# Kernel tuning notes

Measured on AMD Instinct MI355X. Metric: run time of the kernel, lower is better.

## Reference

```python
import jax, jax.numpy as jnp
import numpy as np

D = 4096      # hidden_size
H = 32        # num_attention_heads
DH = 128      # head_dim
DR = 64       # rope_head_dim (rotated suffix of head_dim)
G = 4         # o_groups
QLR = 1536    # q_lora_rank
OLR = 512     # o_lora_rank
WIN = 2048    # window_size
EPS = 1e-6    # norm_eps
THETA = 10000.0


def rms_norm(x, g):
    return x * jax.lax.rsqrt(jnp.mean(x * x, axis=-1, keepdims=True) + EPS) * g


def rope_interleave(x, cos, sin):
    # interleaved (non-neox) rotary: pairs are adjacent even/odd lanes
    x0, x1 = x[..., 0::2], x[..., 1::2]
    r0 = x0 * cos - x1 * sin
    r1 = x0 * sin + x1 * cos
    return jnp.stack([r0, r1], axis=-1).reshape(x.shape)


def setup_inputs() -> dict:
    ks = jax.random.split(jax.random.key(0), 9)
    B, S = 1, 2048
    return {
        "hidden_states": jax.random.normal(ks[0], (B, S, D), jnp.float32),
        "positions": jnp.arange(S, dtype=jnp.int64),
        "wq_a": jax.random.normal(ks[1], (QLR, D), jnp.float32) * 0.02,
        "q_norm_g": jnp.ones((QLR,), jnp.float32),
        "wq_b": jax.random.normal(ks[2], (H * DH, QLR), jnp.float32) * 0.02,
        "wkv": jax.random.normal(ks[3], (DH, D), jnp.float32) * 0.02,
        "kv_norm_g": jnp.ones((DH,), jnp.float32),
        "wo_a": jax.random.normal(ks[4], (G, OLR, (H * DH) // G), jnp.float32) * 0.02,
        "wo_b": jax.random.normal(ks[5], (D, G * OLR), jnp.float32) * 0.02,
        "attn_sink": jax.random.normal(ks[6], (H,), jnp.float32),
    }


def reference(hidden_states, positions, wq_a, q_norm_g, wq_b, wkv, kv_norm_g, wo_a, wo_b, attn_sink):
    B, S, _ = hidden_states.shape
    # low-rank Q path: wq_a -> RMSNorm -> wq_b -> [B,S,H,DH]
    qr = rms_norm(hidden_states @ wq_a.T, q_norm_g)
    q = (qr @ wq_b.T).reshape(B, S, H, DH)
    # shared latent KV (single head_dim vector, MLA/MQA style): wkv -> RMSNorm
    kv = rms_norm(hidden_states @ wkv.T, kv_norm_g)  # [B,S,DH]
    # rotary tables (interleave mode)
    inv_freq = 1.0 / (THETA ** (jnp.arange(0, DR, 2, dtype=jnp.float32) / DR))
    ang = positions.astype(jnp.float32)[:, None] * inv_freq  # [S, DR/2]
    cos, sin = jnp.cos(ang), jnp.sin(ang)
    # rotate last DR dims of q and k
    q = jnp.concatenate(
        [q[..., : DH - DR], rope_interleave(q[..., DH - DR :], cos[None, :, None, :], sin[None, :, None, :])], -1)
    k = jnp.concatenate(
        [kv[..., : DH - DR], rope_interleave(kv[..., DH - DR :], cos[None, :, :], sin[None, :, :])], -1)
    # windowed causal attention with learned per-head sink logit
    scores = jnp.einsum("bshd,btd->bhst", q, k) * (DH ** -0.5)  # [B,H,S,S]
    i = jnp.arange(S)[:, None]
    j = jnp.arange(S)[None, :]
    mask = (j <= i) & ((i - j) < WIN)
    scores = jnp.where(mask[None, None], scores, jnp.finfo(scores.dtype).min)
    sink = jnp.broadcast_to(attn_sink[None, :, None, None], (B, H, S, 1))
    probs = jax.nn.softmax(jnp.concatenate([scores, sink], axis=-1), axis=-1)[..., :S]
    # value = shared normalized latent (pre-rope)
    out = jnp.einsum("bhst,btd->bshd", probs, kv)  # [B,S,H,DH]
    # grouped low-rank output projection: wo_a per group, then wo_b
    out = out.reshape(B, S, G, (H * DH) // G)
    low = jnp.einsum("bsgd,gkd->bsgk", out, wo_a).reshape(B, S, G * OLR)
    return low @ wo_b.T
```

## Files before the change

kernel.cpp:

```cpp
#include <hip/hip_runtime.h>

typedef unsigned short u16;
typedef __bf16 bf16x8 __attribute__((ext_vector_type(8)));
typedef float  f32x4  __attribute__((ext_vector_type(4)));

#define EPSF 1e-6f

__device__ __forceinline__ u16 f2b(float f) {
  unsigned u = __float_as_uint(f);
  u += 0x7fffu + ((u >> 16) & 1u);
  return (u16)(u >> 16);
}
__device__ __forceinline__ float b2f(u16 u) { return __uint_as_float(((unsigned)u) << 16); }
__device__ __forceinline__ u16 f2bh(float f) { return __builtin_bit_cast(u16, (__bf16)f); }

__device__ __forceinline__ unsigned cvtpk(float lo, float hi) {
  unsigned d;
  asm("v_cvt_pk_bf16_f32 %0, %1, %2" : "=v"(d) : "v"(lo), "v"(hi));
  return d;
}

__device__ __forceinline__ void dma16(const u16* g, u16* l) {
  __builtin_amdgcn_global_load_lds(
      (const __attribute__((address_space(1))) unsigned int*)g,
      (__attribute__((address_space(3))) unsigned int*)l, 16, 0, 0);
}

__global__ void dsv4_cvt(const float* __restrict__ hidden, const float* __restrict__ wq_a,
                         const float* __restrict__ wq_b, const float* __restrict__ wkv,
                         const float* __restrict__ wo_a, const float* __restrict__ wo_b,
                         u16* hb, u16* qab, u16* qbb, u16* kvb, u16* oab, u16* obb)
{
  long c = (long)blockIdx.x * 256 + threadIdx.x;
  const float* s; u16* d; long off;
  if      (c < 1048576) { s = hidden; d = hb;  off = c; }
  else if (c < 1835008) { s = wq_a;   d = qab; off = c - 1048576; }
  else if (c < 2621440) { s = wq_b;   d = qbb; off = c - 1835008; }
  else if (c < 2686976) { s = wkv;    d = kvb; off = c - 2621440; }
  else if (c < 2949120) { s = wo_a;   d = oab; off = c - 2686976; }
  else                  { s = wo_b;   d = obb; off = c - 2949120; }
  const float* p = s + off * 8;
  float4 f0 = *(const float4*)p;
  float4 f1 = *(const float4*)(p + 4);
  union { u16 h[8]; int4 v; } u;
  u.h[0] = f2b(f0.x); u.h[1] = f2b(f0.y); u.h[2] = f2b(f0.z); u.h[3] = f2b(f0.w);
  u.h[4] = f2b(f1.x); u.h[5] = f2b(f1.y); u.h[6] = f2b(f1.z); u.h[7] = f2b(f1.w);
  *(int4*)(d + off * 8) = u.v;
}

template<int BM, bool C_F32>
__global__ __launch_bounds__(256, 2)
void dsv4_gemm(const u16* __restrict__ A, int lda, long sAz,
               const u16* __restrict__ B, int ldb, long sBz,
               void* __restrict__ Cv, int ldc, long sCz,
               int K, int splitTile,
               const u16* __restrict__ Baux, void* __restrict__ Caux, int ldcAux)
{
  constexpr int AJ = BM / 32;
  constexpr int NJ = (BM == 128) ? 4 : 2;
  __shared__ __align__(16) u16 As[2 * BM * 64];
  __shared__ __align__(16) u16 Bs[2 * 128 * 64];

  const int tid   = threadIdx.x;
  const int lane  = tid & 63;
  const int qd    = lane >> 4;
  const int l16   = lane & 15;
  const int wid   = tid >> 6;
  const int wbase = tid & 192;
  const int swz   = l16 & 7;

  int n0 = blockIdx.x * 128;
  const int m0 = blockIdx.y * BM;
  void* Cp = Cv;
  if ((int)blockIdx.x >= splitTile) {
    B = Baux; Cp = Caux; ldc = ldcAux;
    n0 = ((int)blockIdx.x - splitTile) * 128;
  }
  A += (long)blockIdx.z * sAz;
  B += (long)blockIdx.z * sBz;

  const u16* gA[AJ]; u16* lA[AJ];
#pragma unroll
  for (int j = 0; j < AJ; j++) {
    int L = j * 256 + tid, row = L >> 3, c = (L & 7) ^ (row & 7);
    gA[j] = A + (long)(m0 + row) * lda + c * 8;
    lA[j] = As + (j * 256 + wbase) * 8;
  }
  const u16* gB[4]; u16* lB[4];
#pragma unroll
  for (int j = 0; j < 4; j++) {
    int L = j * 256 + tid, row = L >> 3, c = (L & 7) ^ (row & 7);
    gB[j] = B + (long)(n0 + row) * ldb + c * 8;
    lB[j] = Bs + (j * 256 + wbase) * 8;
  }

  f32x4 acc[4][NJ];
#pragma unroll
  for (int i = 0; i < 4; i++)
#pragma unroll
    for (int j = 0; j < NJ; j++) { f32x4 z = {0.f, 0.f, 0.f, 0.f}; acc[i][j] = z; }

  const int wm = (BM == 128) ? (wid >> 1) * 64 : 0;
  const int wn = (BM == 128) ? (wid & 1) * 64 : wid * 32;

  auto issue = [&](int s) {
    const int k  = s << 6;
    const int ab = (s & 1) * (BM * 64);
    const int bb = (s & 1) * (128 * 64);
#pragma unroll
    for (int j = 0; j < AJ; j++) dma16(gA[j] + k, lA[j] + ab);
#pragma unroll
    for (int j = 0; j < 4; j++)  dma16(gB[j] + k, lB[j] + bb);
  };

  const int nsteps = K >> 6;
  issue(0);
  asm volatile("s_waitcnt vmcnt(0)" ::: "memory");
  __builtin_amdgcn_s_barrier();

  for (int t = 0; t < nsteps; t++) {
    if (t + 1 < nsteps) issue(t + 1);
    const int ab = (t & 1) * (BM * 64);
    const int bb = (t & 1) * (128 * 64);

#pragma unroll
    for (int ks2 = 0; ks2 < 2; ks2++) {
      bf16x8 af[4], bg[NJ];
#pragma unroll
      for (int i = 0; i < 4; i++) {
        int row = wm + i * 16 + l16;
        af[i] = *(const bf16x8*)&As[ab + row * 64 + ((((ks2 << 2) + qd) ^ swz) << 3)];
      }
#pragma unroll
      for (int j = 0; j < NJ; j++) {
        int row = wn + j * 16 + l16;
        bg[j] = *(const bf16x8*)&Bs[bb + row * 64 + ((((ks2 << 2) + qd) ^ swz) << 3)];
      }
      __builtin_amdgcn_s_setprio(1);
#pragma unroll
      for (int i = 0; i < 4; i++)
#pragma unroll
        for (int j = 0; j < NJ; j++)
          acc[i][j] = __builtin_amdgcn_mfma_f32_16x16x32_bf16(af[i], bg[j], acc[i][j], 0, 0, 0);
      __builtin_amdgcn_s_setprio(0);
    }

    asm volatile("s_waitcnt lgkmcnt(0)" ::: "memory");
    asm volatile("s_waitcnt vmcnt(0)" ::: "memory");
    __builtin_amdgcn_s_barrier();
  }

#pragma unroll
  for (int i = 0; i < 4; i++)
#pragma unroll
    for (int j = 0; j < NJ; j++)
#pragma unroll
      for (int rr = 0; rr < 4; rr++) {
        long row = m0 + wm + i * 16 + qd * 4 + rr;
        int  col = n0 + wn + j * 16 + l16;
        if (C_F32)
          ((float*)Cp)[row * ldc + col + (long)blockIdx.z * sCz] = acc[i][j][rr];
        else
          ((u16*)Cp)[row * ldc + col + (long)blockIdx.z * sCz] = f2b(acc[i][j][rr]);
      }
}

__global__ void dsv4_rmsnorm(const u16* __restrict__ X, const float* __restrict__ g,
                             u16* __restrict__ Y, int W, float invW)
{
  __shared__ float wsum[4];
  const int row = blockIdx.x;
  const u16* x = X + (long)row * W;
  u16* y = Y + (long)row * W;
  float ss = 0.f;
  for (int i = threadIdx.x; i < W; i += 256) { float v = b2f(x[i]); ss += v * v; }
#pragma unroll
  for (int o = 32; o > 0; o >>= 1) ss += __shfl_xor(ss, o);
  const int wid = threadIdx.x >> 6;
  if ((threadIdx.x & 63) == 0) wsum[wid] = ss;
  __syncthreads();
  float tot = wsum[0] + wsum[1] + wsum[2] + wsum[3];
  float scale = rsqrtf(tot * invW + EPSF);
  for (int i = threadIdx.x; i < W; i += 256)
    y[i] = f2b(b2f(x[i]) * scale * g[i]);
}

__global__ void dsv4_kv_finalize(const u16* __restrict__ KVp, const float* __restrict__ g,
                                 u16* __restrict__ Kout, u16* __restrict__ VTout)
{
  const int wid  = threadIdx.x >> 6;
  const int lane = threadIdx.x & 63;
  const int row  = blockIdx.x * 4 + wid;
  const u16* x = KVp + (long)row * 128;
  float x0 = b2f(x[2 * lane]);
  float x1 = b2f(x[2 * lane + 1]);
  float ss = x0 * x0 + x1 * x1;
#pragma unroll
  for (int o = 32; o > 0; o >>= 1) ss += __shfl_xor(ss, o);
  float scale = rsqrtf(ss * (1.f / 128.f) + EPSF);
  float v0 = x0 * scale * g[2 * lane];
  float v1 = x1 * scale * g[2 * lane + 1];
  VTout[(long)(2 * lane) * 2048 + row]     = f2b(v0);
  VTout[(long)(2 * lane + 1) * 2048 + row] = f2b(v1);
  float k0 = v0, k1 = v1;
  if (lane >= 32) {
    int i = lane - 32;
    float invf = powf(10000.f, -(float)i * (1.f / 32.f));
    float sn, cc;
    sincosf((float)row * invf, &sn, &cc);
    k0 = v0 * cc - v1 * sn;
    k1 = v0 * sn + v1 * cc;
  }
  Kout[(long)row * 128 + 2 * lane]     = f2b(k0);
  Kout[(long)row * 128 + 2 * lane + 1] = f2b(k1);
}

__device__ __forceinline__ void attn_step(
    const bf16x8* qf, bool diag, const u16* __restrict__ KsB,
    const u16* __restrict__ VsB,
    int w, int qd, int l16, int swz, float& m, float& negm, float& l, f32x4* o)
{
  const float scl2 = 0.12754245006257017f;
  const float THRU = 62.0f;
  f32x4 st[4];
#pragma unroll
  for (int i = 0; i < 4; i++) { f32x4 z = {0.f, 0.f, 0.f, 0.f}; st[i] = z; }

  __builtin_amdgcn_s_setprio(1);
#pragma unroll
  for (int ks = 0; ks < 4; ks++) {
#pragma unroll
    for (int nt = 0; nt < 4; nt++) {
      int row = nt * 16 + l16;
      bf16x8 bk = *(const bf16x8*)&KsB[row * 128 + ((((ks << 2) + qd) ^ swz) << 3)];
      st[nt] = __builtin_amdgcn_mfma_f32_16x16x32_bf16(bk, qf[ks], st[nt], 0, 0, 0);
    }
  }
  __builtin_amdgcn_s_setprio(0);

  if (diag) {
#pragma unroll
    for (int nt = 0; nt < 4; nt++)
#pragma unroll
      for (int rr = 0; rr < 4; rr++)
        if ((nt * 16 + qd * 4 + rr) > (w * 16 + l16)) st[nt][rr] = -3.0e38f;
  }

  float t0 = fmaxf(fmaxf(st[0][0], st[0][1]), fmaxf(st[0][2], st[0][3]));
  float t1 = fmaxf(fmaxf(st[1][0], st[1][1]), fmaxf(st[1][2], st[1][3]));
  float t2 = fmaxf(fmaxf(st[2][0], st[2][1]), fmaxf(st[2][2], st[2][3]));
  float t3 = fmaxf(fmaxf(st[3][0], st[3][1]), fmaxf(st[3][2], st[3][3]));
  float t = fmaxf(fmaxf(t0, t1), fmaxf(t2, t3));
  t = fmaxf(t, __shfl_xor(t, 16));
  t = fmaxf(t, __shfl_xor(t, 32));

  if (__any(t > m + THRU)) {
    float mn = fmaxf(m, t);
    float aq = exp2f(scl2 * (m - mn));
    m = mn; negm = -scl2 * mn;
    l *= aq;
    float a4[4];
#pragma unroll
    for (int rr = 0; rr < 4; rr++) a4[rr] = __shfl(aq, qd * 4 + rr);
#pragma unroll
    for (int nt = 0; nt < 8; nt++)
#pragma unroll
      for (int rr = 0; rr < 4; rr++) o[nt][rr] *= a4[rr];
  }

#pragma unroll
  for (int nt = 0; nt < 4; nt++)
#pragma unroll
    for (int rr = 0; rr < 4; rr++) {
      float p = exp2f(fmaf(st[nt][rr], scl2, negm));
      l += p;
      st[nt][rr] = p;
    }

  __builtin_amdgcn_s_setprio(1);
#pragma unroll
  for (int ks = 0; ks < 2; ks++) {
    unsigned A0 = cvtpk(st[2 * ks][0],     st[2 * ks][1]);
    unsigned A1 = cvtpk(st[2 * ks][2],     st[2 * ks][3]);
    unsigned B0 = cvtpk(st[2 * ks + 1][0], st[2 * ks + 1][1]);
    unsigned B1 = cvtpk(st[2 * ks + 1][2], st[2 * ks + 1][3]);
    auto s0 = __builtin_amdgcn_permlane32_swap(A0, B0, false, false);
    auto u0 = __builtin_amdgcn_permlane16_swap(s0[0], s0[1], false, false);
    auto s1 = __builtin_amdgcn_permlane32_swap(A1, B1, false, false);
    auto u1 = __builtin_amdgcn_permlane16_swap(s1[0], s1[1], false, false);
    union { unsigned d[4]; bf16x8 v; } ap;
    ap.d[0] = u0[0]; ap.d[1] = u1[0]; ap.d[2] = u0[1]; ap.d[3] = u1[1];
#pragma unroll
    for (int nt = 0; nt < 8; nt++) {
      int row = nt * 16 + l16;
      bf16x8 bv = *(const bf16x8*)&VsB[row * 64 + ((((ks << 2) + qd) ^ swz) << 3)];
      o[nt] = __builtin_amdgcn_mfma_f32_16x16x32_bf16(ap.v, bv, o[nt], 0, 0, 0);
    }
  }
  __builtin_amdgcn_s_setprio(0);
}

__global__ __launch_bounds__(256, 2)
void dsv4_attn(const u16* __restrict__ Q, const u16* __restrict__ Km,
               const u16* __restrict__ VT, const float* __restrict__ sinkp,
               u16* __restrict__ O)
{
  __shared__ __align__(16) u16 Ks[2][64 * 128];
  __shared__ __align__(16) u16 Vs[2][128 * 64];

  const int b  = blockIdx.x;
  const int h  = blockIdx.y;
  const int qtA = 31 - b, qtB = b;
  const int n1 = qtA + 1, nT = n1 + qtB + 1;
  const int tid  = threadIdx.x;
  const int lane = tid & 63;
  const int w    = tid >> 6;
  const int qd   = lane >> 4;
  const int l16  = lane & 15;
  const int swz  = l16 & 7;

  bf16x8 qfA[4], qfB[4];
#pragma unroll
  for (int t = 0; t < 2; t++) {
    int srow = (t ? qtB : qtA) * 64 + w * 16 + l16;
    const u16* qp = Q + (long)srow * 4096 + h * 128 + qd * 8;
    bf16x8* qf = t ? qfB : qfA;
#pragma unroll
    for (int ks = 0; ks < 4; ks++) {
      union { int4 v; u16 hh[8]; } u;
      u.v = *(const int4*)(qp + ks * 32);
      if (ks >= 2) {
#pragma unroll
        for (int j = 0; j < 4; j++) {
          int i = (ks - 2) * 16 + qd * 4 + j;
          float invf = exp2f((float)i * (-13.287712379549449f / 32.f));
          float sn, cc;
          sincosf((float)srow * invf, &sn, &cc);
          float x0 = b2f(u.hh[2 * j]), x1 = b2f(u.hh[2 * j + 1]);
          u.hh[2 * j]     = f2b(x0 * cc - x1 * sn);
          u.hh[2 * j + 1] = f2b(x0 * sn + x1 * cc);
        }
      }
      qf[ks] = *(bf16x8*)&u;
    }
  }

  const u16* gK[4]; const u16* gV[4]; int lKo[4], lVo[4];
#pragma unroll
  for (int j = 0; j < 4; j++) {
    int cl = j * 256 + tid;
    int krow = cl >> 4, kc = (cl & 15) ^ (krow & 7);
    gK[j] = Km + (long)krow * 128 + kc * 8;
    lKo[j] = (j * 256 + (tid & 192)) * 8;
    int vrow = cl >> 3, vc = (cl & 7) ^ (vrow & 7);
    gV[j] = VT + (long)vrow * 2048 + vc * 8;
    lVo[j] = (j * 256 + (tid & 192)) * 8;
  }

  float m = -INFINITY, negm = 0.f, l = 0.f;
  f32x4 o[8];
#pragma unroll
  for (int i = 0; i < 8; i++) { f32x4 z = {0.f, 0.f, 0.f, 0.f}; o[i] = z; }

  const float sink2 = sinkp[h] * 1.4426950408889634f;

#pragma unroll
  for (int j = 0; j < 4; j++) { dma16(gK[j], &Ks[0][lKo[j]]); dma16(gV[j], &Vs[0][lVo[j]]); }

  for (int it = 0; it < nT; ++it) {
    int nxt = it + 1;
    if (nxt < nT) {
      int kt2 = (nxt < n1) ? nxt : nxt - n1;
      int pb = nxt & 1;
#pragma unroll
      for (int j = 0; j < 4; j++) {
        dma16(gK[j] + (long)kt2 * 8192, &Ks[pb][lKo[j]]);
        dma16(gV[j] + (long)kt2 * 64,   &Vs[pb][lVo[j]]);
      }
    }
    asm volatile("s_waitcnt vmcnt(8)" ::: "memory");
    asm volatile("s_barrier" ::: "memory");
    const int cb = it & 1;

    if (it < n1)
      attn_step(qfA, it == n1 - 1, Ks[cb], Vs[cb], w, qd, l16, swz, m, negm, l, o);
    else
      attn_step(qfB, it == nT - 1, Ks[cb], Vs[cb], w, qd, l16, swz, m, negm, l, o);

    asm volatile("s_barrier" ::: "memory");

    if (it == n1 - 1) {
      float ls = l;
      ls += __shfl_xor(ls, 16);
      ls += __shfl_xor(ls, 32);
      float inv = 1.f / (ls + exp2f(sink2 + negm));
      float inv4[4];
#pragma unroll
      for (int rr = 0; rr < 4; rr++) inv4[rr] = __shfl(inv, qd * 4 + rr);
#pragma unroll
      for (int nt = 0; nt < 8; nt++)
#pragma unroll
        for (int rr = 0; rr < 4; rr++)
          O[(long)(qtA * 64 + w * 16 + qd * 4 + rr) * 4096 + h * 128 + nt * 16 + l16] =
              f2bh(o[nt][rr] * inv4[rr]);
      m = -INFINITY; negm = 0.f; l = 0.f;
#pragma unroll
      for (int i = 0; i < 8; i++) { f32x4 z = {0.f, 0.f, 0.f, 0.f}; o[i] = z; }
    }
  }

  {
    float ls = l;
    ls += __shfl_xor(ls, 16);
    ls += __shfl_xor(ls, 32);
    float inv = 1.f / (ls + exp2f(sink2 + negm));
    float inv4[4];
#pragma unroll
    for (int rr = 0; rr < 4; rr++) inv4[rr] = __shfl(inv, qd * 4 + rr);
#pragma unroll
    for (int nt = 0; nt < 8; nt++)
#pragma unroll
      for (int rr = 0; rr < 4; rr++)
        O[(long)(qtB * 64 + w * 16 + qd * 4 + rr) * 4096 + h * 128 + nt * 16 + l16] =
            f2bh(o[nt][rr] * inv4[rr]);
  }
}

extern "C" void kernel_launch(void* const* d_in, const int* in_sizes, int n_in,
                              void* d_out, int out_size, void* d_ws, size_t ws_size,
                              hipStream_t stream)
{
  (void)in_sizes; (void)n_in; (void)out_size; (void)ws_size;
  const float* hidden = (const float*)d_in[0];
  const float* wq_a  = (const float*)d_in[2];
  const float* q_g   = (const float*)d_in[3];
  const float* wq_b  = (const float*)d_in[4];
  const float* wkv   = (const float*)d_in[5];
  const float* kv_g  = (const float*)d_in[6];
  const float* wo_a  = (const float*)d_in[7];
  const float* wo_b  = (const float*)d_in[8];
  const float* sinkp = (const float*)d_in[9];
  float* out = (float*)d_out;

  char* ws = (char*)d_ws;
  u16* hb     = (u16*)(ws);
  u16* low    = (u16*)(ws);
  u16* qab    = (u16*)(ws + (17ul << 20));
  u16* qr     = (u16*)(ws + (17ul << 20));
  u16* qbb    = (u16*)(ws + (30ul << 20));
  u16* kvb    = (u16*)(ws + (43ul << 20));
  u16* oab    = (u16*)(ws + (45ul << 20));
  u16* obb    = (u16*)(ws + (50ul << 20));
  u16* qbuf   = (u16*)(ws + (67ul << 20));
  u16* attnout= (u16*)(ws + (84ul << 20));
  u16* qr_pre = (u16*)(ws + (101ul << 20));
  u16* kvpre  = (u16*)(ws + (108ul << 20));
  u16* kmat   = (u16*)(ws + (108ul << 20) + 524288u);
  u16* vt     = (u16*)(ws + (108ul << 20) + 1048576u);

  const int BIG = 1 << 29;
  dim3 blk(256);

  dsv4_cvt<<<15616, blk, 0, stream>>>(hidden, wq_a, wq_b, wkv, wo_a, wo_b,
                                      hb, qab, qbb, kvb, oab, obb);
  dsv4_gemm<64, false><<<dim3(13, 32, 1), blk, 0, stream>>>(
      hb, 4096, 0, qab, 4096, 0, qr_pre, 1536, 0, 4096, 12, kvb, kvpre, 128);
  dsv4_rmsnorm<<<2048, blk, 0, stream>>>(qr_pre, q_g, qr, 1536, 1.f / 1536.f);
  dsv4_kv_finalize<<<512, blk, 0, stream>>>(kvpre, kv_g, kmat, vt);
  dsv4_gemm<128, false><<<dim3(32, 16, 1), blk, 0, stream>>>(
      qr, 1536, 0, qbb, 1536, 0, qbuf, 4096, 0, 1536, BIG, nullptr, nullptr, 0);
  dsv4_attn<<<dim3(16, 32, 1), blk, 0, stream>>>(qbuf, kmat, vt, sinkp, attnout);
  dsv4_gemm<64, false><<<dim3(4, 32, 4), blk, 0, stream>>>(
      attnout, 4096, 1024, oab, 1024, 524288, low, 2048, 512, 1024, BIG,
      nullptr, nullptr, 0);
  dsv4_gemm<128, true><<<dim3(32, 16, 1), blk, 0, stream>>>(
      low, 2048, 0, obb, 2048, 0, out, 4096, 0, 2048, BIG, nullptr, nullptr, 0);
}
```

Baseline: 386.7 us.

## Split attention blocks per query tile, single-buffer V, raise occupancy

The attention kernel drops the paired-tile scheme (two query tiles per block for load balance) and launches one block per 64-row query tile. V is single-buffered, with its next tile loaded after the PV MFMAs, while K stays double-buffered. This cuts LDS use so launch bounds can allow three blocks per CU. exp2f is replaced by raw v_exp_f32. This trades the balanced work per block for more, shorter blocks, which gives uneven per-block work and exposes V load latency.

```diff
diff --git a/kernel.cpp b/kernel.cpp
--- a/kernel.cpp
+++ b/kernel.cpp
@@ -18,6 +18,9 @@
   unsigned d;
   asm("v_cvt_pk_bf16_f32 %0, %1, %2" : "=v"(d) : "v"(lo), "v"(hi));
   return d;
+}
+__device__ __forceinline__ float fexp2(float x) {
+  float r; asm("v_exp_f32 %0, %1" : "=v"(r) : "v"(x)); return r;
 }
 
 __device__ __forceinline__ void dma16(const u16* g, u16* l) {
@@ -215,103 +218,17 @@
   Kout[(long)row * 128 + 2 * lane + 1] = f2b(k1);
 }
 
-__device__ __forceinline__ void attn_step(
-    const bf16x8* qf, bool diag, const u16* __restrict__ KsB,
-    const u16* __restrict__ VsB,
-    int w, int qd, int l16, int swz, float& m, float& negm, float& l, f32x4* o)
-{
-  const float scl2 = 0.12754245006257017f;
-  const float THRU = 62.0f;
-  f32x4 st[4];
-#pragma unroll
-  for (int i = 0; i < 4; i++) { f32x4 z = {0.f, 0.f, 0.f, 0.f}; st[i] = z; }
-
-  __builtin_amdgcn_s_setprio(1);
-#pragma unroll
-  for (int ks = 0; ks < 4; ks++) {
-#pragma unroll
-    for (int nt = 0; nt < 4; nt++) {
-      int row = nt * 16 + l16;
-      bf16x8 bk = *(const bf16x8*)&KsB[row * 128 + ((((ks << 2) + qd) ^ swz) << 3)];
-      st[nt] = __builtin_amdgcn_mfma_f32_16x16x32_bf16(bk, qf[ks], st[nt], 0, 0, 0);
-    }
-  }
-  __builtin_amdgcn_s_setprio(0);
-
-  if (diag) {
-#pragma unroll
-    for (int nt = 0; nt < 4; nt++)
-#pragma unroll
-      for (int rr = 0; rr < 4; rr++)
-        if ((nt * 16 + qd * 4 + rr) > (w * 16 + l16)) st[nt][rr] = -3.0e38f;
-  }
-
-  float t0 = fmaxf(fmaxf(st[0][0], st[0][1]), fmaxf(st[0][2], st[0][3]));
-  float t1 = fmaxf(fmaxf(st[1][0], st[1][1]), fmaxf(st[1][2], st[1][3]));
-  float t2 = fmaxf(fmaxf(st[2][0], st[2][1]), fmaxf(st[2][2], st[2][3]));
-  float t3 = fmaxf(fmaxf(st[3][0], st[3][1]), fmaxf(st[3][2], st[3][3]));
-  float t = fmaxf(fmaxf(t0, t1), fmaxf(t2, t3));
-  t = fmaxf(t, __shfl_xor(t, 16));
-  t = fmaxf(t, __shfl_xor(t, 32));
-
-  if (__any(t > m + THRU)) {
-    float mn = fmaxf(m, t);
-    float aq = exp2f(scl2 * (m - mn));
-    m = mn; negm = -scl2 * mn;
-    l *= aq;
-    float a4[4];
-#pragma unroll
-    for (int rr = 0; rr < 4; rr++) a4[rr] = __shfl(aq, qd * 4 + rr);
-#pragma unroll
-    for (int nt = 0; nt < 8; nt++)
-#pragma unroll
-      for (int rr = 0; rr < 4; rr++) o[nt][rr] *= a4[rr];
-  }
-
-#pragma unroll
-  for (int nt = 0; nt < 4; nt++)
-#pragma unroll
-    for (int rr = 0; rr < 4; rr++) {
-      float p = exp2f(fmaf(st[nt][rr], scl2, negm));
-      l += p;
-      st[nt][rr] = p;
-    }
-
-  __builtin_amdgcn_s_setprio(1);
-#pragma unroll
-  for (int ks = 0; ks < 2; ks++) {
-    unsigned A0 = cvtpk(st[2 * ks][0],     st[2 * ks][1]);
-    unsigned A1 = cvtpk(st[2 * ks][2],     st[2 * ks][3]);
-    unsigned B0 = cvtpk(st[2 * ks + 1][0], st[2 * ks + 1][1]);
-    unsigned B1 = cvtpk(st[2 * ks + 1][2], st[2 * ks + 1][3]);
-    auto s0 = __builtin_amdgcn_permlane32_swap(A0, B0, false, false);
-    auto u0 = __builtin_amdgcn_permlane16_swap(s0[0], s0[1], false, false);
-    auto s1 = __builtin_amdgcn_permlane32_swap(A1, B1, false, false);
-    auto u1 = __builtin_amdgcn_permlane16_swap(s1[0], s1[1], false, false);
-    union { unsigned d[4]; bf16x8 v; } ap;
-    ap.d[0] = u0[0]; ap.d[1] = u1[0]; ap.d[2] = u0[1]; ap.d[3] = u1[1];
-#pragma unroll
-    for (int nt = 0; nt < 8; nt++) {
-      int row = nt * 16 + l16;
-      bf16x8 bv = *(const bf16x8*)&VsB[row * 64 + ((((ks << 2) + qd) ^ swz) << 3)];
-      o[nt] = __builtin_amdgcn_mfma_f32_16x16x32_bf16(ap.v, bv, o[nt], 0, 0, 0);
-    }
-  }
-  __builtin_amdgcn_s_setprio(0);
-}
-
-__global__ __launch_bounds__(256, 2)
+__global__ __launch_bounds__(256, 3)
 void dsv4_attn(const u16* __restrict__ Q, const u16* __restrict__ Km,
                const u16* __restrict__ VT, const float* __restrict__ sinkp,
                u16* __restrict__ O)
 {
   __shared__ __align__(16) u16 Ks[2][64 * 128];
-  __shared__ __align__(16) u16 Vs[2][128 * 64];
-
-  const int b  = blockIdx.x;
+  __shared__ __align__(16) u16 Vs[128 * 64];
+
+  const int qt = blockIdx.x;
   const int h  = blockIdx.y;
-  const int qtA = 31 - b, qtB = b;
-  const int n1 = qtA + 1, nT = n1 + qtB + 1;
+  const int nT = qt + 1;
   const int tid  = threadIdx.x;
   const int lane = tid & 63;
   const int w    = tid >> 6;
@@ -319,12 +236,13 @@
   const int l16  = lane & 15;
   const int swz  = l16 & 7;
 
-  bf16x8 qfA[4], qfB[4];
-#pragma unroll
-  for (int t = 0; t < 2; t++) {
-    int srow = (t ? qtB : qtA) * 64 + w * 16 + l16;
+  const float scl2 = 0.12754245006257017f;
+  const float THRU = 62.0f;
+
+  bf16x8 qf[4];
+  {
+    int srow = qt * 64 + w * 16 + l16;
     const u16* qp = Q + (long)srow * 4096 + h * 128 + qd * 8;
-    bf16x8* qf = t ? qfB : qfA;
 #pragma unroll
     for (int ks = 0; ks < 4; ks++) {
       union { int4 v; u16 hh[8]; } u;
@@ -365,65 +283,125 @@
   const float sink2 = sinkp[h] * 1.4426950408889634f;
 
 #pragma unroll
-  for (int j = 0; j < 4; j++) { dma16(gK[j], &Ks[0][lKo[j]]); dma16(gV[j], &Vs[0][lVo[j]]); }
+  for (int j = 0; j < 4; j++) dma16(gK[j], &Ks[0][lKo[j]]);
+#pragma unroll
+  for (int j = 0; j < 4; j++) dma16(gV[j], &Vs[lVo[j]]);
 
   for (int it = 0; it < nT; ++it) {
-    int nxt = it + 1;
-    if (nxt < nT) {
-      int kt2 = (nxt < n1) ? nxt : nxt - n1;
-      int pb = nxt & 1;
-#pragma unroll
-      for (int j = 0; j < 4; j++) {
-        dma16(gK[j] + (long)kt2 * 8192, &Ks[pb][lKo[j]]);
-        dma16(gV[j] + (long)kt2 * 64,   &Vs[pb][lVo[j]]);
-      }
-    }
-    asm volatile("s_waitcnt vmcnt(8)" ::: "memory");
+    const bool hn = (it + 1 < nT);
+    if (hn) {
+#pragma unroll
+      for (int j = 0; j < 4; j++)
+        dma16(gK[j] + (long)(it + 1) * 8192, &Ks[(it + 1) & 1][lKo[j]]);
+      asm volatile("s_waitcnt vmcnt(8)" ::: "memory");
+    } else {
+      asm volatile("s_waitcnt vmcnt(4)" ::: "memory");
+    }
     asm volatile("s_barrier" ::: "memory");
-    const int cb = it & 1;
-
-    if (it < n1)
-      attn_step(qfA, it == n1 - 1, Ks[cb], Vs[cb], w, qd, l16, swz, m, negm, l, o);
-    else
-      attn_step(qfB, it == nT - 1, Ks[cb], Vs[cb], w, qd, l16, swz, m, negm, l, o);
-
+
+    const u16* KsB = Ks[it & 1];
+    f32x4 st[4];
+#pragma unroll
+    for (int i = 0; i < 4; i++) { f32x4 z = {0.f, 0.f, 0.f, 0.f}; st[i] = z; }
+
+    __builtin_amdgcn_s_setprio(1);
+#pragma unroll
+    for (int ks = 0; ks < 4; ks++) {
+#pragma unroll
+      for (int nt = 0; nt < 4; nt++) {
+        int row = nt * 16 + l16;
+        bf16x8 bk = *(const bf16x8*)&KsB[row * 128 + ((((ks << 2) + qd) ^ swz) << 3)];
+        st[nt] = __builtin_amdgcn_mfma_f32_16x16x32_bf16(bk, qf[ks], st[nt], 0, 0, 0);
+      }
+    }
+    __builtin_amdgcn_s_setprio(0);
+
+    if (it == nT - 1) {
+#pragma unroll
+      for (int nt = 0; nt < 4; nt++)
+#pragma unroll
+        for (int rr = 0; rr < 4; rr++)
+          if ((nt * 16 + qd * 4 + rr) > (w * 16 + l16)) st[nt][rr] = -3.0e38f;
+    }
+
+    float t0 = fmaxf(fmaxf(st[0][0], st[0][1]), fmaxf(st[0][2], st[0][3]));
+    float t1 = fmaxf(fmaxf(st[1][0], st[1][1]), fmaxf(st[1][2], st[1][3]));
+    float t2 = fmaxf(fmaxf(st[2][0], st[2][1]), fmaxf(st[2][2], st[2][3]));
+    float t3 = fmaxf(fmaxf(st[3][0], st[3][1]), fmaxf(st[3][2], st[3][3]));
+    float t = fmaxf(fmaxf(t0, t1), fmaxf(t2, t3));
+    t = fmaxf(t, __shfl_xor(t, 16));
+    t = fmaxf(t, __shfl_xor(t, 32));
+
+    if (__any(t > m + THRU)) {
+      float mn = fmaxf(m, t);
+      float aq = fexp2(scl2 * (m - mn));
+      m = mn; negm = -scl2 * mn;
+      l *= aq;
+      float a4[4];
+#pragma unroll
+      for (int rr = 0; rr < 4; rr++) a4[rr] = __shfl(aq, qd * 4 + rr);
+#pragma unroll
+      for (int nt = 0; nt < 8; nt++)
+#pragma unroll
+        for (int rr = 0; rr < 4; rr++) o[nt][rr] *= a4[rr];
+    }
+
+#pragma unroll
+    for (int nt = 0; nt < 4; nt++)
+#pragma unroll
+      for (int rr = 0; rr < 4; rr++) {
+        float p = fexp2(fmaf(st[nt][rr], scl2, negm));
+        l += p;
+        st[nt][rr] = p;
+      }
+
+    if (hn) asm volatile("s_waitcnt vmcnt(4)" ::: "memory");
+    else    asm volatile("s_waitcnt vmcnt(0)" ::: "memory");
     asm volatile("s_barrier" ::: "memory");
 
-    if (it == n1 - 1) {
-      float ls = l;
-      ls += __shfl_xor(ls, 16);
-      ls += __shfl_xor(ls, 32);
-      float inv = 1.f / (ls + exp2f(sink2 + negm));
-      float inv4[4];
-#pragma unroll
-      for (int rr = 0; rr < 4; rr++) inv4[rr] = __shfl(inv, qd * 4 + rr);
-#pragma unroll
-      for (int nt = 0; nt < 8; nt++)
-#pragma unroll
-        for (int rr = 0; rr < 4; rr++)
-          O[(long)(qtA * 64 + w * 16 + qd * 4 + rr) * 4096 + h * 128 + nt * 16 + l16] =
-              f2bh(o[nt][rr] * inv4[rr]);
-      m = -INFINITY; negm = 0.f; l = 0.f;
-#pragma unroll
-      for (int i = 0; i < 8; i++) { f32x4 z = {0.f, 0.f, 0.f, 0.f}; o[i] = z; }
-    }
-  }
-
-  {
-    float ls = l;
-    ls += __shfl_xor(ls, 16);
-    ls += __shfl_xor(ls, 32);
-    float inv = 1.f / (ls + exp2f(sink2 + negm));
-    float inv4[4];
-#pragma unroll
-    for (int rr = 0; rr < 4; rr++) inv4[rr] = __shfl(inv, qd * 4 + rr);
-#pragma unroll
-    for (int nt = 0; nt < 8; nt++)
-#pragma unroll
-      for (int rr = 0; rr < 4; rr++)
-        O[(long)(qtB * 64 + w * 16 + qd * 4 + rr) * 4096 + h * 128 + nt * 16 + l16] =
-            f2bh(o[nt][rr] * inv4[rr]);
-  }
+    __builtin_amdgcn_s_setprio(1);
+#pragma unroll
+    for (int ks = 0; ks < 2; ks++) {
+      unsigned A0 = cvtpk(st[2 * ks][0],     st[2 * ks][1]);
+      unsigned A1 = cvtpk(st[2 * ks][2],     st[2 * ks][3]);
+      unsigned B0 = cvtpk(st[2 * ks + 1][0], st[2 * ks + 1][1]);
+      unsigned B1 = cvtpk(st[2 * ks + 1][2], st[2 * ks + 1][3]);
+      auto s0 = __builtin_amdgcn_permlane32_swap(A0, B0, false, false);
+      auto u0 = __builtin_amdgcn_permlane16_swap(s0[0], s0[1], false, false);
+      auto s1 = __builtin_amdgcn_permlane32_swap(A1, B1, false, false);
+      auto u1 = __builtin_amdgcn_permlane16_swap(s1[0], s1[1], false, false);
+      union { unsigned d[4]; bf16x8 v; } ap;
+      ap.d[0] = u0[0]; ap.d[1] = u1[0]; ap.d[2] = u0[1]; ap.d[3] = u1[1];
+#pragma unroll
+      for (int nt = 0; nt < 8; nt++) {
+        int row = nt * 16 + l16;
+        bf16x8 bv = *(const bf16x8*)&Vs[row * 64 + ((((ks << 2) + qd) ^ swz) << 3)];
+        o[nt] = __builtin_amdgcn_mfma_f32_16x16x32_bf16(ap.v, bv, o[nt], 0, 0, 0);
+      }
+    }
+    __builtin_amdgcn_s_setprio(0);
+
+    asm volatile("s_barrier" ::: "memory");
+    if (hn) {
+#pragma unroll
+      for (int j = 0; j < 4; j++)
+        dma16(gV[j] + (long)(it + 1) * 64, &Vs[lVo[j]]);
+    }
+  }
+
+  float ls = l;
+  ls += __shfl_xor(ls, 16);
+  ls += __shfl_xor(ls, 32);
+  float inv = 1.f / (ls + fexp2(sink2 + negm));
+  float inv4[4];
+#pragma unroll
+  for (int rr = 0; rr < 4; rr++) inv4[rr] = __shfl(inv, qd * 4 + rr);
+#pragma unroll
+  for (int nt = 0; nt < 8; nt++)
+#pragma unroll
+    for (int rr = 0; rr < 4; rr++)
+      O[(long)(qt * 64 + w * 16 + qd * 4 + rr) * 4096 + h * 128 + nt * 16 + l16] =
+          f2bh(o[nt][rr] * inv4[rr]);
 }
 
 extern "C" void kernel_launch(void* const* d_in, const int* in_sizes, int n_in,
@@ -469,7 +447,7 @@
   dsv4_kv_finalize<<<512, blk, 0, stream>>>(kvpre, kv_g, kmat, vt);
   dsv4_gemm<128, false><<<dim3(32, 16, 1), blk, 0, stream>>>(
       qr, 1536, 0, qbb, 1536, 0, qbuf, 4096, 0, 1536, BIG, nullptr, nullptr, 0);
-  dsv4_attn<<<dim3(16, 32, 1), blk, 0, stream>>>(qbuf, kmat, vt, sinkp, attnout);
+  dsv4_attn<<<dim3(32, 32, 1), blk, 0, stream>>>(qbuf, kmat, vt, sinkp, attnout);
   dsv4_gemm<64, false><<<dim3(4, 32, 4), blk, 0, stream>>>(
       attnout, 4096, 1024, oab, 1024, 524288, low, 2048, 512, 1024, BIG,
       nullptr, nullptr, 0);
```

After: 415.8 us. +7.5%, slower.
